# Optimization experiments

Hardware: AMD Instinct MI355X
Metric: run time of the kernel (lower is better)

## Reference

```python
import jax, jax.numpy as jnp
import numpy as np

NEG = 1e12  # matches torch's -(1-mask)*1e12 masking constant


def _rope_pointer(qw, kw, mask2d):
    # qw, kw: [B, L, K, H]; mask2d: [B, L, L] bool
    B, L, K, H = qw.shape
    # sinusoidal position embedding, interleaved [sin0,cos0,sin1,cos1,...]
    inv_freq = jnp.power(jnp.float32(10000.0), -2.0 * jnp.arange(H // 2, dtype=jnp.float32) / H)
    ang = jnp.arange(L, dtype=jnp.float32)[:, None] * inv_freq  # [L, H/2]
    cos_pos = jnp.repeat(jnp.cos(ang), 2, axis=-1)[None, :, None, :]  # [1,L,1,H]
    sin_pos = jnp.repeat(jnp.sin(ang), 2, axis=-1)[None, :, None, :]

    def rot(x):
        x2 = jnp.stack([-x[..., 1::2], x[..., ::2]], axis=-1).reshape(x.shape)
        return x * cos_pos + x2 * sin_pos

    q = rot(qw)
    k = rot(kw)
    logits = jnp.einsum('bmhd,bnhd->bhmn', q, k)  # [B,K,L,L]
    m = mask2d[:, None, :, :].astype(logits.dtype)  # [B,1,L,L] broadcasts over K
    return logits * m - (1.0 - m) * NEG


def setup_inputs() -> dict:
    key = jax.random.key(0)
    ks = jax.random.split(key, 8)
    B, L, H = 16, 256, 1024
    tri_hid = arg_hid = eve_hid = 64
    role_num = 60
    scale = 1.0 / np.sqrt(H)
    inp = {
        'cond_bert_embs': jax.random.normal(ks[0], (B, L, H), jnp.float32),
        'tri_W': jax.random.normal(ks[1], (2 * tri_hid, H), jnp.float32) * scale,
        'tri_b': jax.random.normal(ks[2], (2 * tri_hid,), jnp.float32) * 0.01,
        'arg_W': jax.random.normal(ks[3], (2 * arg_hid, H), jnp.float32) * scale,
        'arg_b': jax.random.normal(ks[4], (2 * arg_hid,), jnp.float32) * 0.01,
        'role_W': jax.random.normal(ks[5], (2 * eve_hid * role_num, H), jnp.float32) * scale,
        'role_b': jax.random.normal(ks[6], (2 * eve_hid * role_num,), jnp.float32) * 0.01,
        'word_mask2d': jnp.ones((B, L, L), dtype=bool),
        'triu_mask2d': jnp.triu(jnp.ones((B, L, L), dtype=bool)),
    }
    return inp


def reference(cond_bert_embs, tri_W, tri_b, arg_W, arg_b, role_W, role_b,
              word_mask2d, triu_mask2d):
    B, L, H = cond_bert_embs.shape
    tri_hid = tri_W.shape[0] // 2
    arg_hid = arg_W.shape[0] // 2
    eve_hid = tri_hid  # eve_hid_size == tri_hid_size here
    role_num = role_W.shape[0] // (2 * eve_hid)

    # trigger pointer: K = 1 head
    tri_reps = (cond_bert_embs @ tri_W.T + tri_b).reshape(B, L, 1, 2 * tri_hid)
    tri_qw, tri_kw = jnp.split(tri_reps, 2, axis=-1)
    tri_logits = _rope_pointer(tri_qw, tri_kw, word_mask2d).transpose(0, 2, 3, 1)  # [B,L,L,1]

    # argument pointer: K = 1 head
    arg_reps = (cond_bert_embs @ arg_W.T + arg_b).reshape(B, L, 1, 2 * arg_hid)
    arg_qw, arg_kw = jnp.split(arg_reps, 2, axis=-1)
    arg_logits = _rope_pointer(arg_qw, arg_kw, word_mask2d).transpose(0, 2, 3, 1)  # [B,L,L,1]

    # role pointer: K = role_num heads, upper-triangular mask
    role_reps = (cond_bert_embs @ role_W.T + role_b).reshape(B, L, role_num, 2 * eve_hid)
    role_qw, role_kw = jnp.split(role_reps, 2, axis=-1)
    role_logits = _rope_pointer(role_qw, role_kw, triu_mask2d).transpose(0, 2, 3, 1)
    role_logits = role_logits.reshape(B, L, L, -1, role_num)  # [B,L,L,1,role_num]

    return (tri_logits, arg_logits, role_logits)
```

## Files before the change

### kernel.cpp

```cpp
#include <hip/hip_runtime.h>
#include <hip/hip_bf16.h>
#include <stdint.h>


typedef __attribute__((ext_vector_type(8)))  short short8;
typedef __attribute__((ext_vector_type(4)))  float f32x4;
typedef __attribute__((ext_vector_type(4)))  uint16_t u16x4;

#define LQ    256
#define HID   1024
#define QKS   3968
#define NEGF  (-1000727379968.0f)
#define TA_OFF   1048576ULL
#define ROLE_OFF 2097152ULL

__device__ __forceinline__ uint16_t f2bf(float x) {
  uint32_t u = __builtin_bit_cast(uint32_t, x);
  return (uint16_t)((u + 0x7FFFu + ((u >> 16) & 1u)) >> 16);
}
__device__ __forceinline__ uint16_t f2bf_tr(float x) {
  return (uint16_t)(__builtin_bit_cast(uint32_t, x) >> 16);
}
__device__ __forceinline__ float bf2f(uint16_t b) {
  uint32_t u = ((uint32_t)b) << 16;
  return __builtin_bit_cast(float, u);
}
__device__ __forceinline__ int mask_mode(const void* p) {
  uint32_t w0 = *(const uint32_t*)p;
  if (w0 == 0x01010101u) return 0;
  if (w0 == 1u)          return 1;
  if (w0 == 0x3F803F80u) return 2;
  return 3;
}
__device__ __forceinline__ bool mask_at(const void* p, int mode, size_t idx) {
  if (mode == 0) return ((const uint8_t*)p)[idx] != 0;
  if (mode == 1) return ((const int*)p)[idx] != 0;
  if (mode == 2) return (((const uint16_t*)p)[idx] & 0x7FFFu) != 0;
  return ((const float*)p)[idx] != 0.0f;
}
__device__ __forceinline__ void rope_cs(int pos, float invf, float* s, float* c) {
  float ang = (float)pos * invf;
  __sincosf(ang, s, c);
}
__device__ __forceinline__ float rope_invf(int p) {
  return exp2f(-(float)p * (13.287712379549449f / 32.0f));
}
__device__ __forceinline__ void gload16(const short* g, short* l) {
  __builtin_amdgcn_global_load_lds(
      (const __attribute__((address_space(1))) void*)g,
      (__attribute__((address_space(3))) void*)l, 16, 0, 0);
}

#define EGRP 524288
#define WGRP 1015808
__global__ __launch_bounds__(256)
void k_preconv(const float* __restrict__ E,
               const float* __restrict__ triW, const float* __restrict__ argW,
               const float* __restrict__ roleW,
               short* __restrict__ Eb, short* __restrict__ Wb) {
  for (int gid = blockIdx.x * 256 + threadIdx.x; gid < EGRP + WGRP;
       gid += gridDim.x * 256) {
    const float* src;
    short* dst;
    if (gid < EGRP) {
      src = E + (size_t)gid * 8;
      dst = Eb + (size_t)gid * 8;
    } else {
      int g = gid - EGRP;
      int row = g >> 7;
      int col8 = g & 127;
      const float* srow = (row < 128) ? triW + (size_t)row * HID
                        : (row < 256) ? argW + (size_t)(row - 128) * HID
                                      : roleW + (size_t)(row - 256) * HID;
      src = srow + col8 * 8;
      dst = Wb + (size_t)row * HID + col8 * 8;
    }
    f32x4 v0 = *reinterpret_cast<const f32x4*>(src);
    f32x4 v1 = *reinterpret_cast<const f32x4*>(src + 4);
    short8 r;
    r[0] = (short)f2bf_tr(v0[0]); r[1] = (short)f2bf_tr(v0[1]);
    r[2] = (short)f2bf_tr(v0[2]); r[3] = (short)f2bf_tr(v0[3]);
    r[4] = (short)f2bf_tr(v1[0]); r[5] = (short)f2bf_tr(v1[1]);
    r[6] = (short)f2bf_tr(v1[2]); r[7] = (short)f2bf_tr(v1[3]);
    *reinterpret_cast<short8*>(dst) = r;
  }
}

__global__ __launch_bounds__(256)
void k_proj_pre(const short* __restrict__ Eb, const short* __restrict__ Wb,
                const float* __restrict__ triB, const float* __restrict__ argB,
                const float* __restrict__ roleB,
                short* __restrict__ qs, short* __restrict__ ks, int b0) {
  const int nb = blockIdx.x;
  const int mb = blockIdx.y;
  const int n0 = nb * 128;
  const int mrow0 = b0 * LQ + mb * 128;
  const int lrow0 = mb * 128;

  const float* Bv;
  if (nb == 0)      Bv = triB;
  else if (nb == 1) Bv = argB;
  else              Bv = roleB + (n0 - 256);

  __shared__ short As[2][128 * 32];
  __shared__ short Bs[2][128 * 32];

  const int tid  = threadIdx.x;
  const int lane = tid & 63;
  const int w    = tid >> 6;
  const int wm   = (w >> 1) * 64, wn = (w & 1) * 64;
  const int srr  = lane >> 2;
  const int src8 = (lane & 3) * 8;

  f32x4 acc[4][4] = {};

  auto stage = [&](int buf, int k0) {
#pragma unroll
    for (int cc = 0; cc < 2; ++cc) {
      const int c = w * 2 + cc;
      gload16(Eb + (size_t)(mrow0 + c * 16 + srr) * HID + k0 + src8,
              &As[buf][c * 512]);
      gload16(Wb + (size_t)(n0 + c * 16 + srr) * HID + k0 + src8,
              &Bs[buf][c * 512]);
    }
  };

  stage(0, 0);
  __syncthreads();
  const int NT = HID / 32;
  for (int t = 0; t < NT; ++t) {
    const int buf = t & 1;
    if (t + 1 < NT) stage(buf ^ 1, (t + 1) * 32);
    short8 af[4], bfr[4];
#pragma unroll
    for (int i = 0; i < 4; ++i)
      af[i] = *reinterpret_cast<const short8*>(
          &As[buf][(wm + i * 16 + (lane & 15)) * 32 + (lane >> 4) * 8]);
#pragma unroll
    for (int j = 0; j < 4; ++j)
      bfr[j] = *reinterpret_cast<const short8*>(
          &Bs[buf][(wn + j * 16 + (lane & 15)) * 32 + (lane >> 4) * 8]);
#pragma unroll
    for (int i = 0; i < 4; ++i)
#pragma unroll
      for (int j = 0; j < 4; ++j)
        acc[i][j] = __builtin_amdgcn_mfma_f32_16x16x32_bf16(af[i], bfr[j], acc[i][j], 0, 0, 0);
    __syncthreads();
  }

  const int col_l = lane & 15;
  const int row_h = (lane >> 4) * 4;
#pragma unroll
  for (int j = 0; j < 4; ++j) {
    const int n_loc = wn + j * 16 + col_l;
    const int gcol  = n0 + n_loc;
    const float bias = Bv[n_loc];
    const int d    = gcol & 63;
    const int head = gcol >> 7;
    const bool is_k = (gcol >> 6) & 1;
    const bool odd = d & 1;
    const float invf = rope_invf(d >> 1);
    short* dst = is_k ? ks : qs;
#pragma unroll
    for (int i = 0; i < 4; ++i) {
#pragma unroll
      for (int r = 0; r < 4; ++r) {
        float v  = acc[i][j][r] + bias;
        float vp = __shfl_xor(v, 1, 64);
        int tl  = lrow0 + wm + i * 16 + row_h + r;
        int pos = tl & (LQ - 1);
        float s, c;
        rope_cs(pos, invf, &s, &c);
        float o = odd ? (v * c + vp * s) : (v * c - vp * s);
        dst[(size_t)tl * QKS + head * 64 + d] = (short)f2bf(o);
      }
    }
  }
}

__global__ __launch_bounds__(256)
void k_proj_chunk(const float* __restrict__ E,
                  const float* __restrict__ triW, const float* __restrict__ triB,
                  const float* __restrict__ argW, const float* __restrict__ argB,
                  const float* __restrict__ roleW, const float* __restrict__ roleB,
                  short* __restrict__ qs, short* __restrict__ ks, int b0) {
  const int nb = blockIdx.x;
  const int mb = blockIdx.y;
  const int n0 = nb * 128;
  const int mrow0 = b0 * LQ + mb * 128;
  const int lrow0 = mb * 128;

  const float* W;  const float* Bv;
  if (nb == 0)      { W = triW;                             Bv = triB; }
  else if (nb == 1) { W = argW;                             Bv = argB; }
  else              { W = roleW + (size_t)(n0 - 256) * HID; Bv = roleB + (n0 - 256); }

  __shared__ short As[2][128 * 32];
  __shared__ short Bs[2][128 * 32];

  const int tid  = threadIdx.x;
  const int lane = tid & 63;
  const int w    = tid >> 6;
  const int wm   = (w >> 1) * 64, wn = (w & 1) * 64;
  const int srow = tid >> 2;
  const int scol = (tid & 3) * 8;

  f32x4 acc[4][4] = {};
  f32x4 ra0[2], ra1[2], rb0[2], rb1[2];

  auto load_regs = [&](int k0) {
    const float* pa0 = E + (size_t)(mrow0 + srow) * HID + k0 + scol;
    const float* pa1 = E + (size_t)(mrow0 + 64 + srow) * HID + k0 + scol;
    const float* pb0 = W + (size_t)(srow) * HID + k0 + scol;
    const float* pb1 = W + (size_t)(64 + srow) * HID + k0 + scol;
    ra0[0] = *reinterpret_cast<const f32x4*>(pa0);
    ra0[1] = *reinterpret_cast<const f32x4*>(pa0 + 4);
    ra1[0] = *reinterpret_cast<const f32x4*>(pa1);
    ra1[1] = *reinterpret_cast<const f32x4*>(pa1 + 4);
    rb0[0] = *reinterpret_cast<const f32x4*>(pb0);
    rb0[1] = *reinterpret_cast<const f32x4*>(pb0 + 4);
    rb1[0] = *reinterpret_cast<const f32x4*>(pb1);
    rb1[1] = *reinterpret_cast<const f32x4*>(pb1 + 4);
  };
  auto cvt8 = [&](const f32x4* v) -> short8 {
    short8 r;
    r[0] = (short)f2bf_tr(v[0][0]); r[1] = (short)f2bf_tr(v[0][1]);
    r[2] = (short)f2bf_tr(v[0][2]); r[3] = (short)f2bf_tr(v[0][3]);
    r[4] = (short)f2bf_tr(v[1][0]); r[5] = (short)f2bf_tr(v[1][1]);
    r[6] = (short)f2bf_tr(v[1][2]); r[7] = (short)f2bf_tr(v[1][3]);
    return r;
  };
  auto write_lds = [&](int buf) {
    *reinterpret_cast<short8*>(&As[buf][srow * 32 + scol])        = cvt8(ra0);
    *reinterpret_cast<short8*>(&As[buf][(64 + srow) * 32 + scol]) = cvt8(ra1);
    *reinterpret_cast<short8*>(&Bs[buf][srow * 32 + scol])        = cvt8(rb0);
    *reinterpret_cast<short8*>(&Bs[buf][(64 + srow) * 32 + scol]) = cvt8(rb1);
  };

  load_regs(0); write_lds(0); __syncthreads();
  const int NT = HID / 32;
  for (int t = 0; t < NT; ++t) {
    if (t + 1 < NT) load_regs((t + 1) * 32);
    const int buf = t & 1;
    short8 af[4], bfr[4];
#pragma unroll
    for (int i = 0; i < 4; ++i)
      af[i] = *reinterpret_cast<const short8*>(
          &As[buf][(wm + i * 16 + (lane & 15)) * 32 + (lane >> 4) * 8]);
#pragma unroll
    for (int j = 0; j < 4; ++j)
      bfr[j] = *reinterpret_cast<const short8*>(
          &Bs[buf][(wn + j * 16 + (lane & 15)) * 32 + (lane >> 4) * 8]);
#pragma unroll
    for (int i = 0; i < 4; ++i)
#pragma unroll
      for (int j = 0; j < 4; ++j)
        acc[i][j] = __builtin_amdgcn_mfma_f32_16x16x32_bf16(af[i], bfr[j], acc[i][j], 0, 0, 0);
    __syncthreads();
    if (t + 1 < NT) { write_lds((t + 1) & 1); __syncthreads(); }
  }

  const int col_l = lane & 15;
  const int row_h = (lane >> 4) * 4;
#pragma unroll
  for (int j = 0; j < 4; ++j) {
    const int n_loc = wn + j * 16 + col_l;
    const int gcol  = n0 + n_loc;
    const float bias = Bv[n_loc];
    const int d    = gcol & 63;
    const int head = gcol >> 7;
    const bool is_k = (gcol >> 6) & 1;
    const bool odd = d & 1;
    const float invf = rope_invf(d >> 1);
    short* dst = is_k ? ks : qs;
#pragma unroll
    for (int i = 0; i < 4; ++i) {
#pragma unroll
      for (int r = 0; r < 4; ++r) {
        float v  = acc[i][j][r] + bias;
        float vp = __shfl_xor(v, 1, 64);
        int tl  = lrow0 + wm + i * 16 + row_h + r;
        int pos = tl & (LQ - 1);
        float s, c;
        rope_cs(pos, invf, &s, &c);
        float o = odd ? (v * c + vp * s) : (v * c - vp * s);
        dst[(size_t)tl * QKS + head * 64 + d] = (short)f2bf(o);
      }
    }
  }
}

__global__ __launch_bounds__(512)
void k_role2(const short* __restrict__ qs, const short* __restrict__ ks,
             const void* __restrict__ triu_mask, float* __restrict__ out,
             int b0) {
  const int nt = blockIdx.x, mt = blockIdx.y, bz = blockIdx.z;
  const int bg = b0 + bz;
  const int m0 = mt * 16, n0 = nt * 32;
  __shared__ uint16_t tile[16 * 32 * 60];

  const int tid = threadIdx.x, lane = tid & 63, w = tid >> 6;
  const int frow = lane & 15;
  const int koff = (lane >> 4) * 8;
  const int hstart = (w < 4) ? w * 8 : 32 + (w - 4) * 7;
  const int hcnt   = (w < 4) ? 8 : 7;

  const size_t qbase = ((size_t)bz * LQ + m0) * QKS;
  const size_t kbase = ((size_t)bz * LQ + n0) * QKS;

  for (int i = 0; i < hcnt; ++i) {
    const int r    = hstart + i;
    const int hoff = (2 + r) * 64;
    short8 aq[2], bk[2][2];
#pragma unroll
    for (int kc = 0; kc < 2; ++kc) {
      aq[kc] = *reinterpret_cast<const short8*>(
          qs + qbase + (size_t)frow * QKS + hoff + kc * 32 + koff);
#pragma unroll
      for (int jf = 0; jf < 2; ++jf)
        bk[jf][kc] = *reinterpret_cast<const short8*>(
            ks + kbase + (size_t)(jf * 16 + frow) * QKS + hoff + kc * 32 + koff);
    }
    f32x4 acc[2] = {};
#pragma unroll
    for (int jf = 0; jf < 2; ++jf)
#pragma unroll
      for (int kc = 0; kc < 2; ++kc)
        acc[jf] = __builtin_amdgcn_mfma_f32_16x16x32_bf16(aq[kc], bk[jf][kc], acc[jf], 0, 0, 0);
#pragma unroll
    for (int jf = 0; jf < 2; ++jf)
#pragma unroll
      for (int rg = 0; rg < 4; ++rg) {
        int m = (lane >> 4) * 4 + rg;
        int n = jf * 16 + (lane & 15);
        tile[(m * 32 + n) * 60 + r] = f2bf(acc[jf][rg]);
      }
  }
  __syncthreads();

  const int mode = mask_mode(triu_mask);
  const size_t maskbase = ((size_t)bg * LQ + m0) * LQ + n0;
  const size_t outbase  = ROLE_OFF + (((size_t)bg * LQ + m0) * LQ + n0) * 60;
  for (int f = tid; f < 7680; f += 512) {
    int e  = f * 4;
    int m  = e / 1920;
    int x  = e - m * 1920;
    int n_ = x / 60;
    int rr = x - n_ * 60;
    u16x4 tv = *reinterpret_cast<const u16x4*>(&tile[e]);
    f32x4 v;
    if (rr <= 56) {
      bool mk = mask_at(triu_mask, mode, maskbase + (size_t)m * LQ + n_);
      v[0] = mk ? bf2f(tv[0]) : NEGF;
      v[1] = mk ? bf2f(tv[1]) : NEGF;
      v[2] = mk ? bf2f(tv[2]) : NEGF;
      v[3] = mk ? bf2f(tv[3]) : NEGF;
    } else {
#pragma unroll
      for (int q = 0; q < 4; ++q) {
        int nq = (x + q) / 60;
        bool mk = mask_at(triu_mask, mode, maskbase + (size_t)m * LQ + nq);
        v[q] = mk ? bf2f(tv[q]) : NEGF;
      }
    }
    *reinterpret_cast<f32x4*>(&out[outbase + (size_t)m * (LQ * 60) + x]) = v;
  }
}

__global__ __launch_bounds__(256)
void k_ta_chunk(const short* __restrict__ qs, const short* __restrict__ ks,
                const void* __restrict__ word_mask, float* __restrict__ out,
                int b0) {
  const int mt = blockIdx.x, h = blockIdx.y, bz = blockIdx.z;
  const int bg = b0 + bz;
  const int m0 = mt * 32;
  __shared__ uint16_t tile[32 * 256];

  const int tid = threadIdx.x, lane = tid & 63, w = tid >> 6;
  const int frow = lane & 31;
  const int koff = (lane >> 5) * 8;
  const size_t qbase = ((size_t)bz * LQ + m0) * QKS + h * 64;

  short8 aq[4];
#pragma unroll
  for (int kc = 0; kc < 4; ++kc)
    aq[kc] = *reinterpret_cast<const short8*>(
        qs + qbase + (size_t)frow * QKS + kc * 16 + koff);

  typedef __attribute__((ext_vector_type(16))) float f32x16l;
#pragma unroll
  for (int jn = 0; jn < 2; ++jn) {
    const int ncol0 = w * 64 + jn * 32;
    const size_t kb2 = ((size_t)bz * LQ + ncol0) * QKS + h * 64;
    short8 bk[4];
#pragma unroll
    for (int kc = 0; kc < 4; ++kc)
      bk[kc] = *reinterpret_cast<const short8*>(
          ks + kb2 + (size_t)frow * QKS + kc * 16 + koff);
    f32x16l acc = {};
#pragma unroll
    for (int kc = 0; kc < 4; ++kc)
      acc = __builtin_amdgcn_mfma_f32_32x32x16_bf16(aq[kc], bk[kc], acc, 0, 0, 0);
#pragma unroll
    for (int rg = 0; rg < 16; ++rg) {
      int m = (rg & 3) + 8 * (rg >> 2) + 4 * (lane >> 5);
      int n = ncol0 + (lane & 31);
      tile[m * 256 + n] = f2bf(acc[rg]);
    }
  }
  __syncthreads();

  const int mode = mask_mode(word_mask);
  const size_t maskbase = ((size_t)bg * LQ + m0) * LQ;
  const size_t outbase  = (size_t)h * TA_OFF + ((size_t)bg * LQ + m0) * LQ;
  for (int e = tid; e < 8192; e += 256) {
    int m = e >> 8, n = e & 255;
    bool mk = mask_at(word_mask, mode, maskbase + (size_t)m * LQ + n);
    out[outbase + e] = mk ? bf2f(tile[e]) : NEGF;
  }
}

__global__ __launch_bounds__(256)
void k_ta_fused(const float* __restrict__ E,
                const float* __restrict__ triW, const float* __restrict__ triB,
                const float* __restrict__ argW, const float* __restrict__ argB,
                const void* __restrict__ word_mask, float* __restrict__ out) {
  const int h = blockIdx.x, b = blockIdx.y;
  const float* W  = h ? argW : triW;
  const float* Bv = h ? argB : triB;

  __shared__ short As[2][128 * 32];
  __shared__ short Bs[2][128 * 32];
  __shared__ short qk[256 * 128];

  const int tid  = threadIdx.x;
  const int lane = tid & 63;
  const int w    = tid >> 6;
  const int wm   = (w >> 1) * 64, wn = (w & 1) * 64;
  const int srow = tid >> 2;
  const int scol = (tid & 3) * 8;
  const int col_l = lane & 15;
  const int row_h = (lane >> 4) * 4;

  for (int mi = 0; mi < 2; ++mi) {
    const int r0 = mi * 128;
    f32x4 acc[4][4] = {};
    f32x4 ra0[2], ra1[2], rb0[2], rb1[2];
    auto load_regs = [&](int k0) {
      const float* pa0 = E + ((size_t)b * LQ + r0 + srow) * HID + k0 + scol;
      const float* pa1 = E + ((size_t)b * LQ + r0 + 64 + srow) * HID + k0 + scol;
      const float* pb0 = W + (size_t)(srow) * HID + k0 + scol;
      const float* pb1 = W + (size_t)(64 + srow) * HID + k0 + scol;
      ra0[0] = *reinterpret_cast<const f32x4*>(pa0);
      ra0[1] = *reinterpret_cast<const f32x4*>(pa0 + 4);
      ra1[0] = *reinterpret_cast<const f32x4*>(pa1);
      ra1[1] = *reinterpret_cast<const f32x4*>(pa1 + 4);
      rb0[0] = *reinterpret_cast<const f32x4*>(pb0);
      rb0[1] = *reinterpret_cast<const f32x4*>(pb0 + 4);
      rb1[0] = *reinterpret_cast<const f32x4*>(pb1);
      rb1[1] = *reinterpret_cast<const f32x4*>(pb1 + 4);
    };
    auto cvt8 = [&](const f32x4* v) -> short8 {
      short8 r;
      r[0] = (short)f2bf_tr(v[0][0]); r[1] = (short)f2bf_tr(v[0][1]);
      r[2] = (short)f2bf_tr(v[0][2]); r[3] = (short)f2bf_tr(v[0][3]);
      r[4] = (short)f2bf_tr(v[1][0]); r[5] = (short)f2bf_tr(v[1][1]);
      r[6] = (short)f2bf_tr(v[1][2]); r[7] = (short)f2bf_tr(v[1][3]);
      return r;
    };
    auto write_lds = [&](int buf) {
      *reinterpret_cast<short8*>(&As[buf][srow * 32 + scol])        = cvt8(ra0);
      *reinterpret_cast<short8*>(&As[buf][(64 + srow) * 32 + scol]) = cvt8(ra1);
      *reinterpret_cast<short8*>(&Bs[buf][srow * 32 + scol])        = cvt8(rb0);
      *reinterpret_cast<short8*>(&Bs[buf][(64 + srow) * 32 + scol]) = cvt8(rb1);
    };
    load_regs(0); write_lds(0); __syncthreads();
    for (int t = 0; t < 32; ++t) {
      if (t + 1 < 32) load_regs((t + 1) * 32);
      const int buf = t & 1;
      short8 af[4], bfr[4];
#pragma unroll
      for (int i = 0; i < 4; ++i)
        af[i] = *reinterpret_cast<const short8*>(
            &As[buf][(wm + i * 16 + col_l) * 32 + (lane >> 4) * 8]);
#pragma unroll
      for (int j = 0; j < 4; ++j)
        bfr[j] = *reinterpret_cast<const short8*>(
            &Bs[buf][(wn + j * 16 + col_l) * 32 + (lane >> 4) * 8]);
#pragma unroll
      for (int i = 0; i < 4; ++i)
#pragma unroll
        for (int j = 0; j < 4; ++j)
          acc[i][j] = __builtin_amdgcn_mfma_f32_16x16x32_bf16(af[i], bfr[j], acc[i][j], 0, 0, 0);
      __syncthreads();
      if (t + 1 < 32) { write_lds((t + 1) & 1); __syncthreads(); }
    }
#pragma unroll
    for (int j = 0; j < 4; ++j) {
      const int n_loc = wn + j * 16 + col_l;
      const float bias = Bv[n_loc];
      const int d = n_loc & 63;
      const bool odd = d & 1;
      const float invf = rope_invf(d >> 1);
#pragma unroll
      for (int i = 0; i < 4; ++i) {
#pragma unroll
        for (int r = 0; r < 4; ++r) {
          float v  = acc[i][j][r] + bias;
          float vp = __shfl_xor(v, 1, 64);
          int pos = r0 + wm + i * 16 + row_h + r;
          float s, c;
          rope_cs(pos, invf, &s, &c);
          float o = odd ? (v * c + vp * s) : (v * c - vp * s);
          qk[pos * 128 + n_loc] = (short)f2bf(o);
        }
      }
    }
    __syncthreads();
  }

  const int mode = mask_mode(word_mask);
  short8 aq[4][2];
#pragma unroll
  for (int i = 0; i < 4; ++i)
#pragma unroll
    for (int kk = 0; kk < 2; ++kk)
      aq[i][kk] = *reinterpret_cast<const short8*>(
          &qk[(w * 64 + i * 16 + col_l) * 128 + kk * 32 + (lane >> 4) * 8]);

  for (int ncb = 0; ncb < 4; ++ncb) {
    const int nbase = ncb * 64;
    short8 bk[4][2];
#pragma unroll
    for (int j = 0; j < 4; ++j)
#pragma unroll
      for (int kk = 0; kk < 2; ++kk)
        bk[j][kk] = *reinterpret_cast<const short8*>(
            &qk[(nbase + j * 16 + col_l) * 128 + 64 + kk * 32 + (lane >> 4) * 8]);
    f32x4 acc[4][4] = {};
#pragma unroll
    for (int i = 0; i < 4; ++i)
#pragma unroll
      for (int j = 0; j < 4; ++j)
#pragma unroll
        for (int kk = 0; kk < 2; ++kk)
          acc[i][j] = __builtin_amdgcn_mfma_f32_16x16x32_bf16(aq[i][kk], bk[j][kk], acc[i][j], 0, 0, 0);
#pragma unroll
    for (int i = 0; i < 4; ++i)
#pragma unroll
      for (int j = 0; j < 4; ++j)
#pragma unroll
        for (int r = 0; r < 4; ++r) {
          int gm = w * 64 + i * 16 + row_h + r;
          int gn = nbase + j * 16 + col_l;
          size_t mi_ = ((size_t)b * LQ + gm) * LQ + gn;
          bool mk = mask_at(word_mask, mode, mi_);
          out[(size_t)h * TA_OFF + mi_] = mk ? acc[i][j][r] : NEGF;
        }
  }
}

extern "C" void kernel_launch(void* const* d_in, const int* in_sizes, int n_in,
                              void* d_out, int out_size, void* d_ws, size_t ws_size,
                              hipStream_t stream) {
  (void)in_sizes; (void)n_in; (void)out_size;
  const float* E     = (const float*)d_in[0];
  const float* triW  = (const float*)d_in[1];
  const float* triB  = (const float*)d_in[2];
  const float* argW  = (const float*)d_in[3];
  const float* argB  = (const float*)d_in[4];
  const float* roleW = (const float*)d_in[5];
  const float* roleB = (const float*)d_in[6];
  const void*  wmask = d_in[7];
  const void*  tmask = d_in[8];
  float* out = (float*)d_out;

  const size_t PER_B = (size_t)LQ * QKS * 2 * 2;
  const size_t PRE   = ((size_t)4096 * HID + (size_t)7936 * HID) * 2;

  int cb_pre = (ws_size > PRE) ? (int)((ws_size - PRE) / PER_B) : 0;
  if (cb_pre > 16) cb_pre = 16;

  if (cb_pre >= 1) {
    short* qs = (short*)d_ws;
    short* ks = qs + (size_t)cb_pre * LQ * QKS;
    short* Eb = ks + (size_t)cb_pre * LQ * QKS;
    short* Wb = Eb + (size_t)4096 * HID;
    k_preconv<<<dim3(2048), dim3(256), 0, stream>>>(E, triW, argW, roleW, Eb, Wb);
    for (int b0 = 0; b0 < 16; b0 += cb_pre) {
      int cbi = (16 - b0 < cb_pre) ? (16 - b0) : cb_pre;
      k_proj_pre<<<dim3(62, 2 * cbi), dim3(256), 0, stream>>>(
          Eb, Wb, triB, argB, roleB, qs, ks, b0);
      k_role2<<<dim3(8, 16, cbi), dim3(512), 0, stream>>>(qs, ks, tmask, out, b0);
      k_ta_chunk<<<dim3(8, 2, cbi), dim3(256), 0, stream>>>(qs, ks, wmask, out, b0);
    }
    return;
  }

  int cb = (int)(ws_size / PER_B);
  if (cb > 16) cb = 16;
  if (cb >= 1) {
    short* qs = (short*)d_ws;
    short* ks = qs + (size_t)cb * LQ * QKS;
    for (int b0 = 0; b0 < 16; b0 += cb) {
      int cbi = (16 - b0 < cb) ? (16 - b0) : cb;
      k_proj_chunk<<<dim3(62, 2 * cbi), dim3(256), 0, stream>>>(
          E, triW, triB, argW, argB, roleW, roleB, qs, ks, b0);
      k_role2<<<dim3(8, 16, cbi), dim3(512), 0, stream>>>(qs, ks, tmask, out, b0);
      k_ta_chunk<<<dim3(8, 2, cbi), dim3(256), 0, stream>>>(qs, ks, wmask, out, b0);
    }
  } else {
    short* qs = (short*)d_out;
    short* ks = qs + (size_t)LQ * QKS;
    for (int b0 = 0; b0 < 16; ++b0) {
      k_proj_chunk<<<dim3(62, 2), dim3(256), 0, stream>>>(
          E, triW, triB, argW, argB, roleW, roleB, qs, ks, b0);
      k_role2<<<dim3(8, 16, 1), dim3(512), 0, stream>>>(qs, ks, tmask, out, b0);
    }
    k_ta_fused<<<dim3(2, 16), dim3(256), 0, stream>>>(E, triW, triB, argW, argB,
                                                      wmask, out);
  }
}
```

Before: 272.1 us.

## Use head-major q/k layout and pre-tiled bf16 operands for contiguous loads

Changes the q/k workspace from token-major rows with a 3968-element stride to head-major [batch][head][pos][64] blocks. Each MFMA fragment load in the role and trigger/argument kernels now reads contiguous 128-byte rows instead of widely strided ones. The bf16 preconversion now writes E and W in 16x32 tile-contiguous order, so each projection stage is one contiguous 1KB global-to-LDS load per tile. The role kernel also drops the special case for mask columns that straddle a boundary and unrolls its per-head loop by two. Removing that straddle handling assumes each 4-wide output group never crosses an n boundary, which could be a correctness risk.

```diff
diff --git a/kernel.cpp b/kernel.cpp
--- a/kernel.cpp
+++ b/kernel.cpp
@@ -9,7 +9,8 @@
 
 #define LQ    256
 #define HID   1024
-#define QKS   3968
+#define NH    62
+#define HSTR  16384
 #define NEGF  (-1000727379968.0f)
 #define TA_OFF   1048576ULL
 #define ROLE_OFF 2097152ULL
@@ -63,17 +64,19 @@
     const float* src;
     short* dst;
     if (gid < EGRP) {
-      src = E + (size_t)gid * 8;
-      dst = Eb + (size_t)gid * 8;
+      int row = gid >> 7, col8 = gid & 127;
+      src = E + (size_t)row * HID + col8 * 8;
+      dst = Eb + (((size_t)(row >> 4)) * 32 + (col8 >> 2)) * 512
+               + (row & 15) * 32 + (col8 & 3) * 8;
     } else {
       int g = gid - EGRP;
-      int row = g >> 7;
-      int col8 = g & 127;
+      int row = g >> 7, col8 = g & 127;
       const float* srow = (row < 128) ? triW + (size_t)row * HID
                         : (row < 256) ? argW + (size_t)(row - 128) * HID
                                       : roleW + (size_t)(row - 256) * HID;
       src = srow + col8 * 8;
-      dst = Wb + (size_t)row * HID + col8 * 8;
+      dst = Wb + (((size_t)(row >> 4)) * 32 + (col8 >> 2)) * 512
+               + (row & 15) * 32 + (col8 & 3) * 8;
     }
     f32x4 v0 = *reinterpret_cast<const f32x4*>(src);
     f32x4 v1 = *reinterpret_cast<const f32x4*>(src + 4);
@@ -109,28 +112,26 @@
   const int lane = tid & 63;
   const int w    = tid >> 6;
   const int wm   = (w >> 1) * 64, wn = (w & 1) * 64;
-  const int srr  = lane >> 2;
-  const int src8 = (lane & 3) * 8;
+  const int l8   = lane * 8;
+  const int mt0  = mrow0 >> 4;
+  const int nt0  = n0 >> 4;
 
   f32x4 acc[4][4] = {};
 
-  auto stage = [&](int buf, int k0) {
+  auto stage = [&](int buf, int kt) {
 #pragma unroll
     for (int cc = 0; cc < 2; ++cc) {
       const int c = w * 2 + cc;
-      gload16(Eb + (size_t)(mrow0 + c * 16 + srr) * HID + k0 + src8,
-              &As[buf][c * 512]);
-      gload16(Wb + (size_t)(n0 + c * 16 + srr) * HID + k0 + src8,
-              &Bs[buf][c * 512]);
+      gload16(Eb + ((size_t)(mt0 + c) * 32 + kt) * 512 + l8, &As[buf][c * 512]);
+      gload16(Wb + ((size_t)(nt0 + c) * 32 + kt) * 512 + l8, &Bs[buf][c * 512]);
     }
   };
 
   stage(0, 0);
   __syncthreads();
-  const int NT = HID / 32;
-  for (int t = 0; t < NT; ++t) {
+  for (int t = 0; t < 32; ++t) {
     const int buf = t & 1;
-    if (t + 1 < NT) stage(buf ^ 1, (t + 1) * 32);
+    if (t + 1 < 32) stage(buf ^ 1, t + 1);
     short8 af[4], bfr[4];
 #pragma unroll
     for (int i = 0; i < 4; ++i)
@@ -172,7 +173,8 @@
         float s, c;
         rope_cs(pos, invf, &s, &c);
         float o = odd ? (v * c + vp * s) : (v * c - vp * s);
-        dst[(size_t)tl * QKS + head * 64 + d] = (short)f2bf(o);
+        dst[((size_t)(tl >> 8) * NH + head) * HSTR + (size_t)pos * 64 + d] =
+            (short)f2bf(o);
       }
     }
   }
@@ -284,14 +286,15 @@
         float s, c;
         rope_cs(pos, invf, &s, &c);
         float o = odd ? (v * c + vp * s) : (v * c - vp * s);
-        dst[(size_t)tl * QKS + head * 64 + d] = (short)f2bf(o);
+        dst[((size_t)(tl >> 8) * NH + head) * HSTR + (size_t)pos * 64 + d] =
+            (short)f2bf(o);
       }
     }
   }
 }
 
 __global__ __launch_bounds__(512)
-void k_role2(const short* __restrict__ qs, const short* __restrict__ ks,
+void k_role3(const short* __restrict__ qs, const short* __restrict__ ks,
              const void* __restrict__ triu_mask, float* __restrict__ out,
              int b0) {
   const int nt = blockIdx.x, mt = blockIdx.y, bz = blockIdx.z;
@@ -302,24 +305,19 @@
   const int tid = threadIdx.x, lane = tid & 63, w = tid >> 6;
   const int frow = lane & 15;
   const int koff = (lane >> 4) * 8;
-  const int hstart = (w < 4) ? w * 8 : 32 + (w - 4) * 7;
-  const int hcnt   = (w < 4) ? 8 : 7;
-
-  const size_t qbase = ((size_t)bz * LQ + m0) * QKS;
-  const size_t kbase = ((size_t)bz * LQ + n0) * QKS;
-
-  for (int i = 0; i < hcnt; ++i) {
-    const int r    = hstart + i;
-    const int hoff = (2 + r) * 64;
+  const size_t cbase = (size_t)bz * NH;
+
+  auto do_head = [&](int r) {
+    const size_t hb = (cbase + 2 + r) * HSTR;
     short8 aq[2], bk[2][2];
 #pragma unroll
     for (int kc = 0; kc < 2; ++kc) {
       aq[kc] = *reinterpret_cast<const short8*>(
-          qs + qbase + (size_t)frow * QKS + hoff + kc * 32 + koff);
-#pragma unroll
-      for (int jf = 0; jf < 2; ++jf)
-        bk[jf][kc] = *reinterpret_cast<const short8*>(
-            ks + kbase + (size_t)(jf * 16 + frow) * QKS + hoff + kc * 32 + koff);
+          qs + hb + (size_t)(m0 + frow) * 64 + kc * 32 + koff);
+      bk[0][kc] = *reinterpret_cast<const short8*>(
+          ks + hb + (size_t)(n0 + frow) * 64 + kc * 32 + koff);
+      bk[1][kc] = *reinterpret_cast<const short8*>(
+          ks + hb + (size_t)(n0 + 16 + frow) * 64 + kc * 32 + koff);
     }
     f32x4 acc[2] = {};
 #pragma unroll
@@ -335,6 +333,16 @@
         int n = jf * 16 + (lane & 15);
         tile[(m * 32 + n) * 60 + r] = f2bf(acc[jf][rg]);
       }
+  };
+
+  if (w < 4) {
+    const int h0 = w * 8;
+#pragma unroll 2
+    for (int i = 0; i < 8; ++i) do_head(h0 + i);
+  } else {
+    const int h0 = 32 + (w - 4) * 7;
+#pragma unroll 2
+    for (int i = 0; i < 7; ++i) do_head(h0 + i);
   }
   __syncthreads();
 
@@ -346,23 +354,13 @@
     int m  = e / 1920;
     int x  = e - m * 1920;
     int n_ = x / 60;
-    int rr = x - n_ * 60;
     u16x4 tv = *reinterpret_cast<const u16x4*>(&tile[e]);
+    bool mk = mask_at(triu_mask, mode, maskbase + (size_t)m * LQ + n_);
     f32x4 v;
-    if (rr <= 56) {
-      bool mk = mask_at(triu_mask, mode, maskbase + (size_t)m * LQ + n_);
-      v[0] = mk ? bf2f(tv[0]) : NEGF;
-      v[1] = mk ? bf2f(tv[1]) : NEGF;
-      v[2] = mk ? bf2f(tv[2]) : NEGF;
-      v[3] = mk ? bf2f(tv[3]) : NEGF;
-    } else {
-#pragma unroll
-      for (int q = 0; q < 4; ++q) {
-        int nq = (x + q) / 60;
-        bool mk = mask_at(triu_mask, mode, maskbase + (size_t)m * LQ + nq);
-        v[q] = mk ? bf2f(tv[q]) : NEGF;
-      }
-    }
+    v[0] = mk ? bf2f(tv[0]) : NEGF;
+    v[1] = mk ? bf2f(tv[1]) : NEGF;
+    v[2] = mk ? bf2f(tv[2]) : NEGF;
+    v[3] = mk ? bf2f(tv[3]) : NEGF;
     *reinterpret_cast<f32x4*>(&out[outbase + (size_t)m * (LQ * 60) + x]) = v;
   }
 }
@@ -379,24 +377,23 @@
   const int tid = threadIdx.x, lane = tid & 63, w = tid >> 6;
   const int frow = lane & 31;
   const int koff = (lane >> 5) * 8;
-  const size_t qbase = ((size_t)bz * LQ + m0) * QKS + h * 64;
+  const size_t hb = ((size_t)bz * NH + h) * HSTR;
 
   short8 aq[4];
 #pragma unroll
   for (int kc = 0; kc < 4; ++kc)
     aq[kc] = *reinterpret_cast<const short8*>(
-        qs + qbase + (size_t)frow * QKS + kc * 16 + koff);
+        qs + hb + (size_t)(m0 + frow) * 64 + kc * 16 + koff);
 
   typedef __attribute__((ext_vector_type(16))) float f32x16l;
 #pragma unroll
   for (int jn = 0; jn < 2; ++jn) {
     const int ncol0 = w * 64 + jn * 32;
-    const size_t kb2 = ((size_t)bz * LQ + ncol0) * QKS + h * 64;
     short8 bk[4];
 #pragma unroll
     for (int kc = 0; kc < 4; ++kc)
       bk[kc] = *reinterpret_cast<const short8*>(
-          ks + kb2 + (size_t)frow * QKS + kc * 16 + koff);
+          ks + hb + (size_t)(ncol0 + frow) * 64 + kc * 16 + koff);
     f32x16l acc = {};
 #pragma unroll
     for (int kc = 0; kc < 4; ++kc)
@@ -575,7 +572,7 @@
   const void*  tmask = d_in[8];
   float* out = (float*)d_out;
 
-  const size_t PER_B = (size_t)LQ * QKS * 2 * 2;
+  const size_t PER_B = (size_t)NH * HSTR * 2 * 2;
   const size_t PRE   = ((size_t)4096 * HID + (size_t)7936 * HID) * 2;
 
   int cb_pre = (ws_size > PRE) ? (int)((ws_size - PRE) / PER_B) : 0;
@@ -583,15 +580,15 @@
 
   if (cb_pre >= 1) {
     short* qs = (short*)d_ws;
-    short* ks = qs + (size_t)cb_pre * LQ * QKS;
-    short* Eb = ks + (size_t)cb_pre * LQ * QKS;
+    short* ks = qs + (size_t)cb_pre * NH * HSTR;
+    short* Eb = ks + (size_t)cb_pre * NH * HSTR;
     short* Wb = Eb + (size_t)4096 * HID;
     k_preconv<<<dim3(2048), dim3(256), 0, stream>>>(E, triW, argW, roleW, Eb, Wb);
     for (int b0 = 0; b0 < 16; b0 += cb_pre) {
       int cbi = (16 - b0 < cb_pre) ? (16 - b0) : cb_pre;
       k_proj_pre<<<dim3(62, 2 * cbi), dim3(256), 0, stream>>>(
           Eb, Wb, triB, argB, roleB, qs, ks, b0);
-      k_role2<<<dim3(8, 16, cbi), dim3(512), 0, stream>>>(qs, ks, tmask, out, b0);
+      k_role3<<<dim3(8, 16, cbi), dim3(512), 0, stream>>>(qs, ks, tmask, out, b0);
       k_ta_chunk<<<dim3(8, 2, cbi), dim3(256), 0, stream>>>(qs, ks, wmask, out, b0);
     }
     return;
@@ -601,21 +598,21 @@
   if (cb > 16) cb = 16;
   if (cb >= 1) {
     short* qs = (short*)d_ws;
-    short* ks = qs + (size_t)cb * LQ * QKS;
+    short* ks = qs + (size_t)cb * NH * HSTR;
     for (int b0 = 0; b0 < 16; b0 += cb) {
       int cbi = (16 - b0 < cb) ? (16 - b0) : cb;
       k_proj_chunk<<<dim3(62, 2 * cbi), dim3(256), 0, stream>>>(
           E, triW, triB, argW, argB, roleW, roleB, qs, ks, b0);
-      k_role2<<<dim3(8, 16, cbi), dim3(512), 0, stream>>>(qs, ks, tmask, out, b0);
+      k_role3<<<dim3(8, 16, cbi), dim3(512), 0, stream>>>(qs, ks, tmask, out, b0);
       k_ta_chunk<<<dim3(8, 2, cbi), dim3(256), 0, stream>>>(qs, ks, wmask, out, b0);
     }
   } else {
     short* qs = (short*)d_out;
-    short* ks = qs + (size_t)LQ * QKS;
+    short* ks = qs + (size_t)NH * HSTR;
     for (int b0 = 0; b0 < 16; ++b0) {
       k_proj_chunk<<<dim3(62, 2), dim3(256), 0, stream>>>(
           E, triW, triB, argW, argB, roleW, roleB, qs, ks, b0);
-      k_role2<<<dim3(8, 16, 1), dim3(512), 0, stream>>>(qs, ks, tmask, out, b0);
+      k_role3<<<dim3(8, 16, 1), dim3(512), 0, stream>>>(qs, ks, tmask, out, b0);
     }
     k_ta_fused<<<dim3(2, 16), dim3(256), 0, stream>>>(E, triW, triB, argW, argB,
                                                       wmask, out);
```

After: 269.9 us. About the same (-0.8%).
